# Performance work log

Hardware: AMD Instinct MI355X
Metric: run time of the kernel (lower is better)

The kernel has to match this reference:

```python
import jax, jax.numpy as jnp
import numpy as np

NUM_USERS = 100000
NUM_ITEMS = 50000
N_NODES = NUM_USERS + NUM_ITEMS
EMBED_DIM = 64
NUM_LAYERS = 3
N_EDGES = 1000000


def setup_inputs() -> dict:
    key = jax.random.key(0)
    k1, k2 = jax.random.split(key)
    edge_index = jax.random.randint(k1, (2, N_EDGES), 0, N_NODES, dtype=jnp.int64)
    # xavier_uniform for Embedding weight [N, d]
    limit = float(np.sqrt(6.0 / (N_NODES + EMBED_DIM)))
    emb_weight = jax.random.uniform(k2, (N_NODES, EMBED_DIM), dtype=jnp.float32,
                                    minval=-limit, maxval=limit)
    return {"edge_index": edge_index, "emb_weight": emb_weight}


def _lgconv(x, src, dst, norm):
    # out[dst] += norm * x[src]  (degree-normalized scatter-add)
    msgs = x[src] * norm[:, None]              # [E, d]
    return jax.ops.segment_sum(msgs, dst, num_segments=N_NODES)


def reference(edge_index, emb_weight):
    src, dst = edge_index[0], edge_index[1]
    # gcn_norm with add_self_loops=False: deg over target (col) index
    deg = jax.ops.segment_sum(jnp.ones((N_EDGES,), emb_weight.dtype), dst,
                              num_segments=N_NODES)
    dinv = jnp.where(deg > 0, jax.lax.rsqrt(jnp.maximum(deg, 1.0)), 0.0)
    norm = dinv[src] * dinv[dst]               # [E]

    emb = emb_weight
    acc = emb                                   # running sum over layer outputs
    for _ in range(NUM_LAYERS):
        emb = _lgconv(emb, src, dst, norm)
        acc = acc + emb
    out = acc / (NUM_LAYERS + 1)                # mean over stacked layer embeddings
    user_emb = out[:NUM_USERS]
    item_emb = out[NUM_USERS:]
    return (user_emb, item_emb)
```

## Files before the change

kernel.cpp:

```cpp
#include <hip/hip_runtime.h>
#include <hip/hip_fp16.h>


constexpr int kNodes     = 150000;
constexpr int kDim       = 64;
constexpr int kEdges     = 1000000;
constexpr int kEmbFloats = kNodes * kDim;
constexpr int kBkt       = (kNodes + 255) / 256;
constexpr int kBktCap    = 2048;
constexpr int kChunk     = 4096;

typedef float  floatx4 __attribute__((ext_vector_type(4)));

__device__ __forceinline__ int wave_incl_scan(int v, int lane) {
    #pragma unroll
    for (int s = 1; s < 64; s <<= 1) {
        int u = __shfl_up(v, s);
        if (lane >= s) v += u;
    }
    return v;
}

#define ACC_LO(s, r) asm("v_fma_mix_f32 %0, %1, 1.0, %0 op_sel:[0,0,0] op_sel_hi:[1,0,0]" : "+v"(s) : "v"(r))
#define ACC_HI(s, r) asm("v_fma_mix_f32 %0, %1, 1.0, %0 op_sel:[1,0,0] op_sel_hi:[1,0,0]" : "+v"(s) : "v"(r))

#define ACC_ROW(rr) do { \
    ACC_LO(s0, rr.x); ACC_HI(s1, rr.x); \
    ACC_LO(s2, rr.y); ACC_HI(s3, rr.y); \
    ACC_LO(s4, rr.z); ACC_HI(s5, rr.z); \
    ACC_LO(s6, rr.w); ACC_HI(s7, rr.w); } while (0)


__global__ __launch_bounds__(1024) void binA_kernel(const int* __restrict__ src,
                                                    const int* __restrict__ dst,
                                                    int* __restrict__ cur,
                                                    unsigned* __restrict__ bin) {
    __shared__ int hist[1024];
    __shared__ int cursor[1024];
    __shared__ int sexcl[1024];
    __shared__ int gstart[1024];
    __shared__ int wsum[16];
    __shared__ unsigned staged[kChunk];
    __shared__ unsigned short sbkt[kChunk];

    int t      = threadIdx.x;
    int lane   = t & 63;
    int w      = t >> 6;
    int chunk0 = blockIdx.x * kChunk;
    int n      = min(kChunk, kEdges - chunk0);

    hist[t] = 0;
    __syncthreads();

    int myb[4], myd[4];
    #pragma unroll
    for (int j = 0; j < 4; ++j) {
        int i = j * 1024 + t;
        if (i < n) {
            int d = dst[chunk0 + i];
            myb[j] = d >> 8;
            myd[j] = d & 255;
            atomicAdd(&hist[myb[j]], 1);
        } else myb[j] = -1;
    }
    __syncthreads();

    int c   = hist[t];
    int inc = wave_incl_scan(c, lane);
    if (lane == 63) wsum[w] = inc;
    __syncthreads();
    if (w == 0) {
        int v  = (lane < 16) ? wsum[lane] : 0;
        int sc = wave_incl_scan(v, lane);
        if (lane < 16) wsum[lane] = sc - v;
    }
    __syncthreads();
    int excl = wsum[w] + inc - c;
    sexcl[t]  = excl;
    cursor[t] = excl;
    if (t < kBkt) gstart[t] = atomicAdd(&cur[t], c);
    __syncthreads();

    #pragma unroll
    for (int j = 0; j < 4; ++j) {
        int i = j * 1024 + t;
        if (i < n) {
            int s = src[chunk0 + i];
            unsigned pk = ((unsigned)myd[j] << 24) | (unsigned)s;
            int p = atomicAdd(&cursor[myb[j]], 1);
            staged[p] = pk;
            sbkt[p]   = (unsigned short)myb[j];
        }
    }
    __syncthreads();

    #pragma unroll
    for (int j = 0; j < 4; ++j) {
        int i = j * 1024 + t;
        if (i < n) {
            int bu = sbkt[i];
            int gp = gstart[bu] + (i - sexcl[bu]);
            if (gp < kBktCap) bin[(size_t)bu * kBktCap + gp] = staged[i];
        }
    }
}


__global__ __launch_bounds__(1024) void scan_base_kernel(const int* __restrict__ cur,
                                                         int* __restrict__ base) {
    __shared__ int wsum[16];
    int t = threadIdx.x;
    int lane = t & 63, w = t >> 6;
    int v = (t < kBkt) ? min(cur[t], kBktCap) : 0;
    int inc = wave_incl_scan(v, lane);
    if (lane == 63) wsum[w] = inc;
    __syncthreads();
    if (w == 0) {
        int x  = (lane < 16) ? wsum[lane] : 0;
        int sc = wave_incl_scan(x, lane);
        if (lane < 16) wsum[lane] = sc - x;
    }
    __syncthreads();
    if (t < kBkt) base[t] = wsum[w] + inc - v;
}


__global__ __launch_bounds__(256) void binB_kernel(const int* __restrict__ cur,
                                                   const int* __restrict__ base,
                                                   const unsigned* __restrict__ bin,
                                                   int* __restrict__ pairs,
                                                   int2* __restrict__ offcnt,
                                                   float* __restrict__ dinv,
                                                   const float4* __restrict__ emb4,
                                                   int4* __restrict__ y4) {
    __shared__ int lcnt[256];
    __shared__ int cursor[256];
    __shared__ int wsum[4];
    __shared__ int stage[kBktCap];
    __shared__ float sdinv[256];

    int b = blockIdx.x;
    int t = threadIdx.x;
    int lane = t & 63, w = t >> 6;
    int cnt = min(cur[b], kBktCap);
    int bs  = base[b];
    const unsigned* mybin = bin + (size_t)b * kBktCap;

    lcnt[t] = 0;
    __syncthreads();
    for (int i = t; i < cnt; i += 256) atomicAdd(&lcnt[mybin[i] >> 24], 1);
    __syncthreads();

    int c   = lcnt[t];
    int inc = wave_incl_scan(c, lane);
    if (lane == 63) wsum[w] = inc;
    __syncthreads();
    if (t == 0) {
        int a = 0;
        #pragma unroll
        for (int k = 0; k < 4; ++k) { int v = wsum[k]; wsum[k] = a; a += v; }
    }
    __syncthreads();
    int excl = wsum[w] + inc - c;

    int node = (b << 8) + t;
    float dv = (c > 0) ? rsqrtf((float)c) : 0.0f;
    sdinv[t] = dv;
    if (node < kNodes) {
        offcnt[node] = make_int2(bs + excl, c);
        dinv[node]   = dv;
    }
    cursor[t] = excl;
    __syncthreads();

    for (int i = t; i < cnt; i += 256) {
        unsigned v = mybin[i];
        int p = atomicAdd(&cursor[v >> 24], 1);
        stage[p] = (int)(v & 0x00FFFFFFu);
    }
    __syncthreads();
    for (int i = t; i < cnt; i += 256) pairs[bs + i] = stage[i];

    #pragma unroll
    for (int k = 0; k < 8; ++k) {
        int idx   = (k << 8) + t;
        int nl    = idx >> 3;
        int node2 = (b << 8) + nl;
        int qq    = idx & 7;
        if (node2 < kNodes) {
            float d = sdinv[nl];
            size_t e = (size_t)node2 * 16 + (size_t)qq * 2;
            float4 v0 = emb4[e];
            float4 v1 = emb4[e + 1];
            __half2 p0 = __floats2half2_rn(v0.x * d, v0.y * d);
            __half2 p1 = __floats2half2_rn(v0.z * d, v0.w * d);
            __half2 p2 = __floats2half2_rn(v1.x * d, v1.y * d);
            __half2 p3 = __floats2half2_rn(v1.z * d, v1.w * d);
            int4 wv;
            wv.x = *reinterpret_cast<int*>(&p0); wv.y = *reinterpret_cast<int*>(&p1);
            wv.z = *reinterpret_cast<int*>(&p2); wv.w = *reinterpret_cast<int*>(&p3);
            y4[(size_t)node2 * 8 + qq] = wv;
        } else if (node2 == kNodes) {
            int4 z; z.x = 0; z.y = 0; z.z = 0; z.w = 0;
            y4[(size_t)node2 * 8 + qq] = z;
        }
    }
}


__global__ __launch_bounds__(256) void gather_kernel(const int2* __restrict__ offcnt,
                                                     const int* __restrict__ pairs,
                                                     const __half* __restrict__ x16,
                                                     const float* __restrict__ dinv,
                                                     __half* __restrict__ yOut,
                                                     const float4* __restrict__ emb4,
                                                     const __half* __restrict__ y1,
                                                     const __half* __restrict__ y2,
                                                     float* __restrict__ outf,
                                                     int mode) {
    int t    = blockIdx.x * 256 + threadIdx.x;
    int node = t >> 3;
    if (node > kNodes) return;
    int q    = t & 7;
    if (node == kNodes) {
        if (mode == 0) {
            int4 z; z.x = 0; z.y = 0; z.z = 0; z.w = 0;
            ((int4*)(yOut + ((size_t)node << 6)))[q] = z;
        }
        return;
    }
    int lane = threadIdx.x & 63;
    int gb   = lane & 56;

    int2 oc = offcnt[node];
    int b = oc.x, cnt = oc.y;

    float s0 = 0.f, s1 = 0.f, s2 = 0.f, s3 = 0.f,
          s4 = 0.f, s5 = 0.f, s6 = 0.f, s7 = 0.f;

    int mysrc = (q < cnt) ? pairs[b + q] : kNodes;
    for (int base2 = 0; base2 < cnt; base2 += 8) {
        int np  = base2 + 8 + q;
        int nxt = (np < cnt) ? pairs[b + np] : kNodes;

        int si0 = __shfl(mysrc, gb + 0);
        int si1 = __shfl(mysrc, gb + 1);
        int si2 = __shfl(mysrc, gb + 2);
        int si3 = __shfl(mysrc, gb + 3);
        int si4 = __shfl(mysrc, gb + 4);
        int si5 = __shfl(mysrc, gb + 5);
        int si6 = __shfl(mysrc, gb + 6);
        int si7 = __shfl(mysrc, gb + 7);
        int4 r0 = *(const int4*)(x16 + ((size_t)si0 << 6) + (q << 3));
        int4 r1 = *(const int4*)(x16 + ((size_t)si1 << 6) + (q << 3));
        int4 r2 = *(const int4*)(x16 + ((size_t)si2 << 6) + (q << 3));
        int4 r3 = *(const int4*)(x16 + ((size_t)si3 << 6) + (q << 3));
        int4 r4 = *(const int4*)(x16 + ((size_t)si4 << 6) + (q << 3));
        int4 r5 = *(const int4*)(x16 + ((size_t)si5 << 6) + (q << 3));
        int4 r6 = *(const int4*)(x16 + ((size_t)si6 << 6) + (q << 3));
        int4 r7 = *(const int4*)(x16 + ((size_t)si7 << 6) + (q << 3));
        ACC_ROW(r0); ACC_ROW(r1); ACC_ROW(r2); ACC_ROW(r3);
        ACC_ROW(r4); ACC_ROW(r5); ACC_ROW(r6); ACC_ROW(r7);
        mysrc = nxt;
    }

    float dv = dinv[node];
    if (mode == 0) {
        float dv2 = dv * dv;
        __half2 p0 = __floats2half2_rn(s0 * dv2, s1 * dv2);
        __half2 p1 = __floats2half2_rn(s2 * dv2, s3 * dv2);
        __half2 p2 = __floats2half2_rn(s4 * dv2, s5 * dv2);
        __half2 p3 = __floats2half2_rn(s6 * dv2, s7 * dv2);
        int4 wv;
        wv.x = *reinterpret_cast<int*>(&p0); wv.y = *reinterpret_cast<int*>(&p1);
        wv.z = *reinterpret_cast<int*>(&p2); wv.w = *reinterpret_cast<int*>(&p3);
        ((int4*)(yOut + ((size_t)node << 6)))[q] = wv;
    } else {
        float sq = sqrtf((float)cnt);
        size_t i4 = (size_t)node * 16 + (size_t)q * 2;
        int4 r1 = ((const int4*)(y1 + ((size_t)node << 6)))[q];
        int4 r2 = ((const int4*)(y2 + ((size_t)node << 6)))[q];
        float4 e0 = emb4[i4];
        float4 e1 = emb4[i4 + 1];
        float2 a0 = __half22float2(*reinterpret_cast<__half2*>(&r1.x));
        float2 a1 = __half22float2(*reinterpret_cast<__half2*>(&r1.y));
        float2 a2 = __half22float2(*reinterpret_cast<__half2*>(&r1.z));
        float2 a3 = __half22float2(*reinterpret_cast<__half2*>(&r1.w));
        float2 c0 = __half22float2(*reinterpret_cast<__half2*>(&r2.x));
        float2 c1 = __half22float2(*reinterpret_cast<__half2*>(&r2.y));
        float2 c2 = __half22float2(*reinterpret_cast<__half2*>(&r2.z));
        float2 c3 = __half22float2(*reinterpret_cast<__half2*>(&r2.w));
        floatx4 o0, o1;
        o0.x = (e0.x + (a0.x + c0.x) * sq + s0 * dv) * 0.25f;
        o0.y = (e0.y + (a0.y + c0.y) * sq + s1 * dv) * 0.25f;
        o0.z = (e0.z + (a1.x + c1.x) * sq + s2 * dv) * 0.25f;
        o0.w = (e0.w + (a1.y + c1.y) * sq + s3 * dv) * 0.25f;
        o1.x = (e1.x + (a2.x + c2.x) * sq + s4 * dv) * 0.25f;
        o1.y = (e1.y + (a2.y + c2.y) * sq + s5 * dv) * 0.25f;
        o1.z = (e1.z + (a3.x + c3.x) * sq + s6 * dv) * 0.25f;
        o1.w = (e1.w + (a3.y + c3.y) * sq + s7 * dv) * 0.25f;
        floatx4* op = (floatx4*)(outf + i4 * 4);
        __builtin_nontemporal_store(o0, op);
        __builtin_nontemporal_store(o1, op + 1);
    }
}


extern "C" void kernel_launch(void* const* d_in, const int* in_sizes, int n_in,
                              void* d_out, int out_size, void* d_ws, size_t ws_size,
                              hipStream_t stream) {
    const int*   edge  = (const int*)d_in[0];
    const int*   src   = edge;
    const int*   dst   = edge + kEdges;
    const float* emb_w = (const float*)d_in[1];
    float*       out   = (float*)d_out;

    char*     ws      = (char*)d_ws;
    int*      cur     = (int*)(ws);
    int*      binBase = (int*)(ws + 4096);
    int2*     offcnt  = (int2*)(ws + 8192);
    float*    dinv    = (float*)(ws + 1208192);
    int*      pairs   = (int*)(ws + 1808192);
    unsigned* bin     = (unsigned*)(ws + 5808192);
    __half*   y0      = (__half*)(ws + 10608704);
    __half*   yA      = (__half*)(ws + 29808832);
    __half*   yB      = (__half*)(ws + 49008960);

    const int binABlocks   = (kEdges + kChunk - 1) / kChunk;
    const int gatherBlocks = ((kNodes + 1) * 8 + 255) / 256;

    (void)hipMemsetAsync(cur, 0, (size_t)kBkt * 4, stream);
    binA_kernel<<<binABlocks, 1024, 0, stream>>>(src, dst, cur, bin);
    scan_base_kernel<<<1, 1024, 0, stream>>>(cur, binBase);
    binB_kernel<<<kBkt, 256, 0, stream>>>(cur, binBase, bin, pairs, offcnt, dinv,
                                          (const float4*)emb_w, (int4*)y0);

    gather_kernel<<<gatherBlocks, 256, 0, stream>>>(offcnt, pairs, y0, dinv,
                                                    yA, nullptr, nullptr, nullptr,
                                                    nullptr, 0);
    gather_kernel<<<gatherBlocks, 256, 0, stream>>>(offcnt, pairs, yA, dinv,
                                                    yB, nullptr, nullptr, nullptr,
                                                    nullptr, 0);
    gather_kernel<<<gatherBlocks, 256, 0, stream>>>(offcnt, pairs, yB, dinv,
                                                    nullptr, (const float4*)emb_w,
                                                    yA, yB, out, 1);
}
```

Measured before the change: 234.4 us.

## Degree-sort nodes within buckets for gather balance and fold scan into binB

Each binB block now builds a counting-sort permutation of its 256 nodes by in-degree, capped at 63. The gather kernels visit nodes in that order, so the 8-node groups in a wave have similar edge counts and less divergent loop trip counts. The separate single-block scan kernel is removed: each binB block computes its own base offset by summing the counts of earlier buckets. The dinv array is dropped and recomputed from cnt in the gather. The cost is a redundant prefix reduction in every binB block, an extra indirection through order, and scattered output writes.

```diff
diff --git a/kernel.cpp b/kernel.cpp
--- a/kernel.cpp
+++ b/kernel.cpp
@@ -106,36 +106,18 @@
 }
 
 
-__global__ __launch_bounds__(1024) void scan_base_kernel(const int* __restrict__ cur,
-                                                         int* __restrict__ base) {
-    __shared__ int wsum[16];
-    int t = threadIdx.x;
-    int lane = t & 63, w = t >> 6;
-    int v = (t < kBkt) ? min(cur[t], kBktCap) : 0;
-    int inc = wave_incl_scan(v, lane);
-    if (lane == 63) wsum[w] = inc;
-    __syncthreads();
-    if (w == 0) {
-        int x  = (lane < 16) ? wsum[lane] : 0;
-        int sc = wave_incl_scan(x, lane);
-        if (lane < 16) wsum[lane] = sc - x;
-    }
-    __syncthreads();
-    if (t < kBkt) base[t] = wsum[w] + inc - v;
-}
-
-
 __global__ __launch_bounds__(256) void binB_kernel(const int* __restrict__ cur,
-                                                   const int* __restrict__ base,
                                                    const unsigned* __restrict__ bin,
                                                    int* __restrict__ pairs,
                                                    int2* __restrict__ offcnt,
-                                                   float* __restrict__ dinv,
+                                                   int* __restrict__ order,
                                                    const float4* __restrict__ emb4,
                                                    int4* __restrict__ y4) {
     __shared__ int lcnt[256];
     __shared__ int cursor[256];
     __shared__ int wsum[4];
+    __shared__ int wred[4];
+    __shared__ int chist[64];
     __shared__ int stage[kBktCap];
     __shared__ float sdinv[256];
 
@@ -143,18 +125,36 @@
     int t = threadIdx.x;
     int lane = t & 63, w = t >> 6;
     int cnt = min(cur[b], kBktCap);
-    int bs  = base[b];
     const unsigned* mybin = bin + (size_t)b * kBktCap;
 
+    {
+        int acc = 0;
+        for (int j = t; j < b; j += 256) acc += min(cur[j], kBktCap);
+        #pragma unroll
+        for (int s = 32; s; s >>= 1) acc += __shfl_down(acc, s);
+        if (lane == 0) wred[w] = acc;
+    }
+
     lcnt[t] = 0;
-    __syncthreads();
+    if (t < 64) chist[t] = 0;
+    __syncthreads();
+    int bs = wred[0] + wred[1] + wred[2] + wred[3];
+
     for (int i = t; i < cnt; i += 256) atomicAdd(&lcnt[mybin[i] >> 24], 1);
     __syncthreads();
 
     int c   = lcnt[t];
     int inc = wave_incl_scan(c, lane);
     if (lane == 63) wsum[w] = inc;
-    __syncthreads();
+    int cv = min(c, 63);
+    atomicAdd(&chist[cv], 1);
+    __syncthreads();
+
+    if (t < 64) {
+        int v  = chist[t];
+        int sc = wave_incl_scan(v, lane);
+        chist[t] = sc - v;
+    }
     if (t == 0) {
         int a = 0;
         #pragma unroll
@@ -166,11 +166,13 @@
     int node = (b << 8) + t;
     float dv = (c > 0) ? rsqrtf((float)c) : 0.0f;
     sdinv[t] = dv;
-    if (node < kNodes) {
-        offcnt[node] = make_int2(bs + excl, c);
-        dinv[node]   = dv;
-    }
+    if (node < kNodes) offcnt[node] = make_int2(bs + excl, c);
     cursor[t] = excl;
+
+    {
+        int slot = atomicAdd(&chist[cv], 1);
+        order[(b << 8) + slot] = (node < kNodes) ? node : kNodes;
+    }
     __syncthreads();
 
     for (int i = t; i < cnt; i += 256) {
@@ -209,9 +211,9 @@
 
 
 __global__ __launch_bounds__(256) void gather_kernel(const int2* __restrict__ offcnt,
+                                                     const int* __restrict__ order,
                                                      const int* __restrict__ pairs,
                                                      const __half* __restrict__ x16,
-                                                     const float* __restrict__ dinv,
                                                      __half* __restrict__ yOut,
                                                      const float4* __restrict__ emb4,
                                                      const __half* __restrict__ y1,
@@ -219,13 +221,13 @@
                                                      float* __restrict__ outf,
                                                      int mode) {
     int t    = blockIdx.x * 256 + threadIdx.x;
-    int node = t >> 3;
-    if (node > kNodes) return;
+    int slot = t >> 3;
     int q    = t & 7;
+    int node = order[slot];
     if (node == kNodes) {
         if (mode == 0) {
             int4 z; z.x = 0; z.y = 0; z.z = 0; z.w = 0;
-            ((int4*)(yOut + ((size_t)node << 6)))[q] = z;
+            ((int4*)(yOut + ((size_t)kNodes << 6)))[q] = z;
         }
         return;
     }
@@ -264,7 +266,7 @@
         mysrc = nxt;
     }
 
-    float dv = dinv[node];
+    float dv = (cnt > 0) ? rsqrtf((float)cnt) : 0.0f;
     if (mode == 0) {
         float dv2 = dv * dv;
         __half2 p0 = __floats2half2_rn(s0 * dv2, s1 * dv2);
@@ -317,31 +319,29 @@
 
     char*     ws      = (char*)d_ws;
     int*      cur     = (int*)(ws);
-    int*      binBase = (int*)(ws + 4096);
-    int2*     offcnt  = (int2*)(ws + 8192);
-    float*    dinv    = (float*)(ws + 1208192);
-    int*      pairs   = (int*)(ws + 1808192);
-    unsigned* bin     = (unsigned*)(ws + 5808192);
-    __half*   y0      = (__half*)(ws + 10608704);
-    __half*   yA      = (__half*)(ws + 29808832);
-    __half*   yB      = (__half*)(ws + 49008960);
+    int*      order   = (int*)(ws + 4096);
+    int2*     offcnt  = (int2*)(ws + 604160);
+    int*      pairs   = (int*)(ws + 1804160);
+    unsigned* bin     = (unsigned*)(ws + 5804160);
+    __half*   y0      = (__half*)(ws + 10604672);
+    __half*   yA      = (__half*)(ws + 29804800);
+    __half*   yB      = (__half*)(ws + 49004928);
 
     const int binABlocks   = (kEdges + kChunk - 1) / kChunk;
-    const int gatherBlocks = ((kNodes + 1) * 8 + 255) / 256;
+    const int gatherBlocks = (kBkt * 256 * 8) / 256;
 
     (void)hipMemsetAsync(cur, 0, (size_t)kBkt * 4, stream);
     binA_kernel<<<binABlocks, 1024, 0, stream>>>(src, dst, cur, bin);
-    scan_base_kernel<<<1, 1024, 0, stream>>>(cur, binBase);
-    binB_kernel<<<kBkt, 256, 0, stream>>>(cur, binBase, bin, pairs, offcnt, dinv,
+    binB_kernel<<<kBkt, 256, 0, stream>>>(cur, bin, pairs, offcnt, order,
                                           (const float4*)emb_w, (int4*)y0);
 
-    gather_kernel<<<gatherBlocks, 256, 0, stream>>>(offcnt, pairs, y0, dinv,
+    gather_kernel<<<gatherBlocks, 256, 0, stream>>>(offcnt, order, pairs, y0,
                                                     yA, nullptr, nullptr, nullptr,
                                                     nullptr, 0);
-    gather_kernel<<<gatherBlocks, 256, 0, stream>>>(offcnt, pairs, yA, dinv,
+    gather_kernel<<<gatherBlocks, 256, 0, stream>>>(offcnt, order, pairs, yA,
                                                     yB, nullptr, nullptr, nullptr,
                                                     nullptr, 0);
-    gather_kernel<<<gatherBlocks, 256, 0, stream>>>(offcnt, pairs, yB, dinv,
+    gather_kernel<<<gatherBlocks, 256, 0, stream>>>(offcnt, order, pairs, yB,
                                                     nullptr, (const float4*)emb_w,
                                                     yA, yB, out, 1);
 }
```

New measurement: 218.4 us. -6.8%, faster.
